# Performance work log

Measured on AMD Instinct MI355X. Metric: run time of the kernel, lower is better.

## Reference

```python
import jax, jax.numpy as jnp
import numpy as np

B, W, H, C = 64, 32, 32, 64
K = 4096  # embedding_length


def setup_inputs() -> dict:
    key = jax.random.key(0)
    k1, k2 = jax.random.split(key)
    encoded = jax.random.normal(k1, (B, W, H, C), dtype=jnp.float32)
    # tf.random.uniform init in the original
    codebook = jax.random.uniform(k2, (K, C), dtype=jnp.float32)
    return {"encoded": encoded, "codebook": codebook}


def reference(encoded, codebook):
    b, w, h, c = encoded.shape
    x = encoded.reshape(b * w * h, c)  # [N, c]
    # the tiled tf.pow(x - e, 2).sum(-1), without the [N, K, c] intermediate).
    x_sq = jnp.sum(x * x, axis=-1, keepdims=True)          # [N, 1]
    e_sq = jnp.sum(codebook * codebook, axis=-1)           # [K]
    dist = x_sq - 2.0 * (x @ codebook.T) + e_sq[None, :]   # [N, K]
    idx = jnp.argmin(dist, axis=-1)                        # [N]
    q = codebook[idx].reshape(b, w, h, c)                  # gather
    # Straight-through estimator as in the original forward
    out = encoded + jax.lax.stop_gradient(q - encoded)
    return out, idx.reshape(b, w, h)
```

## Files before the change

### kernel.cpp

```cpp
#include <hip/hip_runtime.h>


#define NPTS    65536
#define CDIM    64
#define KCODES  4096
#define WAVES   4
#define KPW     (KCODES / WAVES)
#define TILES   (KPW / 16)
#define PADC    64
#define LISTCAP 8192
#define DELTA   0.25f

typedef __attribute__((ext_vector_type(8))) short short8;
typedef __attribute__((ext_vector_type(4))) float f32x4;

__device__ __forceinline__ unsigned short f2bf(float x) {
    unsigned u = __float_as_uint(x);
    return (unsigned short)((u + 0x7FFFu + ((u >> 16) & 1u)) >> 16);
}

struct BT { short8 b0, b1; float hh; };

__global__ __launch_bounds__(256) void vq_prep(const float* __restrict__ cb,
                                               short* __restrict__ cbb,
                                               float* __restrict__ h) {
    int k = blockIdx.x * 256 + threadIdx.x;
    const float4* p = reinterpret_cast<const float4*>(cb + (size_t)k * CDIM);
    float s0 = 0.f, s1 = 0.f, s2 = 0.f, s3 = 0.f;
#pragma unroll
    for (int i = 0; i < 16; i += 2) {
        float4 va = p[i], vb = p[i + 1];
        s0 = fmaf(va.x, va.x, s0); s1 = fmaf(va.y, va.y, s1);
        s2 = fmaf(va.z, va.z, s2); s3 = fmaf(va.w, va.w, s3);
        s0 = fmaf(vb.x, vb.x, s0); s1 = fmaf(vb.y, vb.y, s1);
        s2 = fmaf(vb.z, vb.z, s2); s3 = fmaf(vb.w, vb.w, s3);
        short8 o;
        o[0] = (short)f2bf(va.x); o[1] = (short)f2bf(va.y);
        o[2] = (short)f2bf(va.z); o[3] = (short)f2bf(va.w);
        o[4] = (short)f2bf(vb.x); o[5] = (short)f2bf(vb.y);
        o[6] = (short)f2bf(vb.z); o[7] = (short)f2bf(vb.w);
        *reinterpret_cast<short8*>(cbb + (size_t)k * CDIM + i * 4) = o;
    }
    h[k] = 0.5f * ((s0 + s1) + (s2 + s3));
}

__global__ __launch_bounds__(256) void vq_main(const float* __restrict__ enc,
                                               const float* __restrict__ cbf,
                                               const short* __restrict__ cbb,
                                               const float* __restrict__ h,
                                               float* __restrict__ out) {
    __shared__ unsigned list[LISTCAP];
    __shared__ float rowmax[WAVES][64];
    __shared__ float thrL[64];
    __shared__ unsigned long long mkey[64];
    __shared__ unsigned lcnt;

    const int tid  = threadIdx.x;
    const int wid  = tid >> 6, lane = tid & 63;
    const int lrow = lane & 15, lseg = lane >> 4;
    const int pbase = blockIdx.x * 64;
    const int k0 = wid * KPW;

    if (tid == 0) lcnt = 0;
    if (tid < 64) mkey[tid] = ~0ull;

    short8 afr[4][2];
#pragma unroll
    for (int rt = 0; rt < 4; ++rt)
#pragma unroll
        for (int kk = 0; kk < 2; ++kk) {
            const float4* xp = reinterpret_cast<const float4*>(
                enc + (size_t)(pbase + rt * 16 + lrow) * CDIM + kk * 32 + lseg * 8);
            float4 v0 = xp[0], v1 = xp[1];
            short8 a;
            a[0] = (short)f2bf(v0.x); a[1] = (short)f2bf(v0.y);
            a[2] = (short)f2bf(v0.z); a[3] = (short)f2bf(v0.w);
            a[4] = (short)f2bf(v1.x); a[5] = (short)f2bf(v1.y);
            a[6] = (short)f2bf(v1.z); a[7] = (short)f2bf(v1.w);
            afr[rt][kk] = a;
        }
    __syncthreads();

    auto loadB = [&](int ct, BT& s) {
        int code = k0 + ct * 16 + lrow;
        const short* base = cbb + (size_t)code * CDIM + lseg * 8;
        s.b0 = *reinterpret_cast<const short8*>(base);
        s.b1 = *reinterpret_cast<const short8*>(base + 32);
        s.hh = h[code];
    };

    f32x4 best[4];
#pragma unroll
    for (int rt = 0; rt < 4; ++rt)
#pragma unroll
        for (int i = 0; i < 4; ++i) best[rt][i] = -__builtin_inff();

    {
        BT s0, s1, s2, s3;
        loadB(0, s0); loadB(8, s1); loadB(16, s2); loadB(24, s3);
#define SSBODY(SLOT, J)                                                        \
        {                                                                      \
            float nh = -SLOT.hh;                                               \
            f32x4 acc[4];                                                      \
            _Pragma("unroll")                                                  \
            for (int rt = 0; rt < 4; ++rt) {                                   \
                acc[rt][0] = nh; acc[rt][1] = nh;                              \
                acc[rt][2] = nh; acc[rt][3] = nh;                              \
            }                                                                  \
            _Pragma("unroll")                                                  \
            for (int rt = 0; rt < 4; ++rt)                                     \
                acc[rt] = __builtin_amdgcn_mfma_f32_16x16x32_bf16(afr[rt][0], SLOT.b0, acc[rt], 0, 0, 0); \
            _Pragma("unroll")                                                  \
            for (int rt = 0; rt < 4; ++rt)                                     \
                acc[rt] = __builtin_amdgcn_mfma_f32_16x16x32_bf16(afr[rt][1], SLOT.b1, acc[rt], 0, 0, 0); \
            _Pragma("unroll")                                                  \
            for (int rt = 0; rt < 4; ++rt)                                     \
                _Pragma("unroll")                                              \
                for (int i = 0; i < 4; ++i)                                    \
                    best[rt][i] = fmaxf(best[rt][i], acc[rt][i]);              \
            loadB((((J) + 4) & 7) * 8, SLOT);                                  \
        }
        SSBODY(s0, 0) SSBODY(s1, 1) SSBODY(s2, 2) SSBODY(s3, 3)
        SSBODY(s0, 4) SSBODY(s1, 5) SSBODY(s2, 6) SSBODY(s3, 7)
#undef SSBODY
    }

#pragma unroll
    for (int m = 1; m <= 8; m <<= 1)
#pragma unroll
        for (int rt = 0; rt < 4; ++rt)
#pragma unroll
            for (int i = 0; i < 4; ++i)
                best[rt][i] = fmaxf(best[rt][i], __shfl_xor(best[rt][i], m, 64));
    if (lrow == 0) {
#pragma unroll
        for (int rt = 0; rt < 4; ++rt)
#pragma unroll
            for (int i = 0; i < 4; ++i)
                rowmax[wid][rt * 16 + lseg * 4 + i] = best[rt][i];
    }
    __syncthreads();
    if (tid < 64) {
        float m0 = fmaxf(rowmax[0][tid], rowmax[1][tid]);
        float m1 = fmaxf(rowmax[2][tid], rowmax[3][tid]);
        thrL[tid] = fmaxf(m0, m1) - DELTA;
    }
    __syncthreads();

    f32x4 mthr[4];
#pragma unroll
    for (int rt = 0; rt < 4; ++rt)
#pragma unroll
        for (int i = 0; i < 4; ++i) mthr[rt][i] = -thrL[rt * 16 + lseg * 4 + i];

    {
        BT s0, s1, s2, s3;
        loadB(0, s0); loadB(1, s1); loadB(2, s2); loadB(3, s3);
#define S2BODY(SLOT, T)                                                        \
        {                                                                      \
            f32x4 acc[4];                                                      \
            _Pragma("unroll")                                                  \
            for (int rt = 0; rt < 4; ++rt)                                     \
                acc[rt] = __builtin_amdgcn_mfma_f32_16x16x32_bf16(afr[rt][0], SLOT.b0, mthr[rt], 0, 0, 0); \
            _Pragma("unroll")                                                  \
            for (int rt = 0; rt < 4; ++rt)                                     \
                acc[rt] = __builtin_amdgcn_mfma_f32_16x16x32_bf16(afr[rt][1], SLOT.b1, acc[rt], 0, 0, 0); \
            float hh = SLOT.hh;                                                \
            unsigned mask = 0u;                                                \
            _Pragma("unroll")                                                  \
            for (int rt = 0; rt < 4; ++rt)                                     \
                _Pragma("unroll")                                              \
                for (int i = 0; i < 4; ++i)                                    \
                    mask |= (acc[rt][i] >= hh) ? (1u << (rt * 4 + i)) : 0u;    \
            if (mask) {                                                        \
                unsigned code = (unsigned)(k0 + (T) * 16 + lrow);              \
                do {                                                           \
                    int kz = __builtin_ctz(mask);                              \
                    mask &= mask - 1u;                                         \
                    unsigned row = ((unsigned)(kz >> 2) << 4)                  \
                                 + (unsigned)(lseg * 4) + (unsigned)(kz & 3);   \
                    unsigned pos = atomicAdd(&lcnt, 1u);                       \
                    if (pos < LISTCAP) list[pos] = (row << 12) | code;         \
                } while (mask);                                                \
            }                                                                  \
            loadB((T) + 4, SLOT);           \
        }
        for (int t = 0; t < TILES; t += 4) {
            S2BODY(s0, t + 0)
            S2BODY(s1, t + 1)
            S2BODY(s2, t + 2)
            S2BODY(s3, t + 3)
        }
#undef S2BODY
    }
    __syncthreads();

    unsigned cnt = lcnt; if (cnt > LISTCAP) cnt = LISTCAP;
    for (unsigned t4 = tid; t4 < cnt * 4; t4 += 256) {
        unsigned t = t4 >> 2; int q = t4 & 3;
        unsigned e = list[t];
        int row = (int)(e >> 12), c = (int)(e & 4095u);
        const float4* xp = reinterpret_cast<const float4*>(enc + (size_t)(pbase + row) * CDIM) + q * 4;
        const float4* ep = reinterpret_cast<const float4*>(cbf + (size_t)c * CDIM) + q * 4;
        float a0 = 0.f, a1 = 0.f, a2 = 0.f, a3 = 0.f;
#pragma unroll
        for (int i = 0; i < 4; ++i) {
            float4 xv = xp[i], ev = ep[i];
            a0 = fmaf(xv.x, ev.x, a0); a1 = fmaf(xv.y, ev.y, a1);
            a2 = fmaf(xv.z, ev.z, a2); a3 = fmaf(xv.w, ev.w, a3);
        }
        float p = (a0 + a1) + (a2 + a3);
        p += __shfl_xor(p, 1, 64);
        p += __shfl_xor(p, 2, 64);
        if (q == 0) {
            float d2 = fmaf(-2.f, p, 2.f * h[c]);
            unsigned bb = __float_as_uint(d2);
            unsigned ord = bb ^ (unsigned)(((int)bb >> 31) | 0x80000000);
            atomicMin(&mkey[row], ((unsigned long long)ord << 32) | (unsigned)c);
        }
    }
    __syncthreads();

    {
        int p = tid >> 2, q = tid & 3;
        int c = (int)(mkey[p] & 4095u);
        const float4* ep = reinterpret_cast<const float4*>(cbf + (size_t)c * CDIM) + q * 4;
        float4* op = reinterpret_cast<float4*>(out + (size_t)(pbase + p) * CDIM) + q * 4;
#pragma unroll
        for (int i = 0; i < 4; ++i) op[i] = ep[i];
        if (tid < 64)
            out[(size_t)NPTS * CDIM + pbase + tid] = (float)(mkey[tid] & 4095u);
    }
}

extern "C" void kernel_launch(void* const* d_in, const int* in_sizes, int n_in,
                              void* d_out, int out_size, void* d_ws, size_t ws_size,
                              hipStream_t stream) {
    const float* enc = (const float*)d_in[0];
    const float* cb  = (const float*)d_in[1];
    float* out = (float*)d_out;

    short* cbb = (short*)d_ws;
    float* hws = (float*)(cbb + (size_t)(KCODES + PADC) * CDIM);

    vq_prep<<<KCODES / 256, 256, 0, stream>>>(cb, cbb, hws);
    vq_main<<<NPTS / 64, 256, 0, stream>>>(enc, cb, cbb, hws, out);
}
```

Baseline: 134.0 us.

## Switch to 32x32x16 MFMA tiles with 32 points per block

Replaces the 16x16x32 bf16 MFMA tiling (64 points per block, four row tiles) with 32x32x16 MFMA over 32 points per block and 32 codes per tile, and doubles the grid size. This cuts A-fragment registers and changes the reduction, threshold and row mapping to match the new accumulator layout. The goal is better MFMA throughput per instruction and more blocks for occupancy. The cost is that codebook B fragments are now reloaded by twice as many blocks, and the software pipeline depth drops from four slots to two.

Result: slower. 177.5 us (+32.5%).

```diff
diff --git a/kernel.cpp b/kernel.cpp
--- a/kernel.cpp
+++ b/kernel.cpp
@@ -5,21 +5,22 @@
 #define CDIM    64
 #define KCODES  4096
 #define WAVES   4
+#define PPB     32
 #define KPW     (KCODES / WAVES)
-#define TILES   (KPW / 16)
+#define TILES   (KPW / 32)
 #define PADC    64
-#define LISTCAP 8192
+#define LISTCAP 4096
 #define DELTA   0.25f
 
 typedef __attribute__((ext_vector_type(8))) short short8;
-typedef __attribute__((ext_vector_type(4))) float f32x4;
+typedef __attribute__((ext_vector_type(16))) float f32x16;
 
 __device__ __forceinline__ unsigned short f2bf(float x) {
     unsigned u = __float_as_uint(x);
     return (unsigned short)((u + 0x7FFFu + ((u >> 16) & 1u)) >> 16);
 }
 
-struct BT { short8 b0, b1; float hh; };
+struct BT { short8 b[4]; float hh; };
 
 __global__ __launch_bounds__(256) void vq_prep(const float* __restrict__ cb,
                                                short* __restrict__ cbb,
@@ -50,146 +51,144 @@
                                                const float* __restrict__ h,
                                                float* __restrict__ out) {
     __shared__ unsigned list[LISTCAP];
-    __shared__ float rowmax[WAVES][64];
-    __shared__ float thrL[64];
-    __shared__ unsigned long long mkey[64];
+    __shared__ float rowmax[WAVES][PPB];
+    __shared__ float thrL[PPB];
+    __shared__ unsigned long long mkey[PPB];
     __shared__ unsigned lcnt;
 
     const int tid  = threadIdx.x;
     const int wid  = tid >> 6, lane = tid & 63;
-    const int lrow = lane & 15, lseg = lane >> 4;
-    const int pbase = blockIdx.x * 64;
+    const int col  = lane & 31, hs = lane >> 5;
+    const int pbase = blockIdx.x * PPB;
     const int k0 = wid * KPW;
 
     if (tid == 0) lcnt = 0;
-    if (tid < 64) mkey[tid] = ~0ull;
-
-    short8 afr[4][2];
-#pragma unroll
-    for (int rt = 0; rt < 4; ++rt)
-#pragma unroll
-        for (int kk = 0; kk < 2; ++kk) {
-            const float4* xp = reinterpret_cast<const float4*>(
-                enc + (size_t)(pbase + rt * 16 + lrow) * CDIM + kk * 32 + lseg * 8);
-            float4 v0 = xp[0], v1 = xp[1];
-            short8 a;
-            a[0] = (short)f2bf(v0.x); a[1] = (short)f2bf(v0.y);
-            a[2] = (short)f2bf(v0.z); a[3] = (short)f2bf(v0.w);
-            a[4] = (short)f2bf(v1.x); a[5] = (short)f2bf(v1.y);
-            a[6] = (short)f2bf(v1.z); a[7] = (short)f2bf(v1.w);
-            afr[rt][kk] = a;
-        }
-    __syncthreads();
-
-    auto loadB = [&](int ct, BT& s) {
-        int code = k0 + ct * 16 + lrow;
-        const short* base = cbb + (size_t)code * CDIM + lseg * 8;
-        s.b0 = *reinterpret_cast<const short8*>(base);
-        s.b1 = *reinterpret_cast<const short8*>(base + 32);
+    if (tid < PPB) mkey[tid] = ~0ull;
+
+    short8 afr[4];
+#pragma unroll
+    for (int c = 0; c < 4; ++c) {
+        const float4* xp = reinterpret_cast<const float4*>(
+            enc + (size_t)(pbase + col) * CDIM + c * 16 + hs * 8);
+        float4 v0 = xp[0], v1 = xp[1];
+        short8 a;
+        a[0] = (short)f2bf(v0.x); a[1] = (short)f2bf(v0.y);
+        a[2] = (short)f2bf(v0.z); a[3] = (short)f2bf(v0.w);
+        a[4] = (short)f2bf(v1.x); a[5] = (short)f2bf(v1.y);
+        a[6] = (short)f2bf(v1.z); a[7] = (short)f2bf(v1.w);
+        afr[c] = a;
+    }
+    __syncthreads();
+
+    auto loadB = [&](int t, BT& s) {
+        int code = k0 + t * 32 + col;
+        const short* base = cbb + (size_t)code * CDIM + hs * 8;
+#pragma unroll
+        for (int c = 0; c < 4; ++c)
+            s.b[c] = *reinterpret_cast<const short8*>(base + c * 16);
         s.hh = h[code];
     };
 
-    f32x4 best[4];
-#pragma unroll
-    for (int rt = 0; rt < 4; ++rt)
-#pragma unroll
-        for (int i = 0; i < 4; ++i) best[rt][i] = -__builtin_inff();
+    auto mfmaT = [&](const BT& s, const f32x16& cin) -> f32x16 {
+        f32x16 acc = __builtin_amdgcn_mfma_f32_32x32x16_bf16(afr[0], s.b[0], cin, 0, 0, 0);
+        acc = __builtin_amdgcn_mfma_f32_32x32x16_bf16(afr[1], s.b[1], acc, 0, 0, 0);
+        acc = __builtin_amdgcn_mfma_f32_32x32x16_bf16(afr[2], s.b[2], acc, 0, 0, 0);
+        acc = __builtin_amdgcn_mfma_f32_32x32x16_bf16(afr[3], s.b[3], acc, 0, 0, 0);
+        return acc;
+    };
+
+    float best[16];
+#pragma unroll
+    for (int r = 0; r < 16; ++r) best[r] = -__builtin_inff();
 
     {
-        BT s0, s1, s2, s3;
-        loadB(0, s0); loadB(8, s1); loadB(16, s2); loadB(24, s3);
-#define SSBODY(SLOT, J)                                                        \
-        {                                                                      \
-            float nh = -SLOT.hh;                                               \
-            f32x4 acc[4];                                                      \
-            _Pragma("unroll")                                                  \
-            for (int rt = 0; rt < 4; ++rt) {                                   \
-                acc[rt][0] = nh; acc[rt][1] = nh;                              \
-                acc[rt][2] = nh; acc[rt][3] = nh;                              \
-            }                                                                  \
-            _Pragma("unroll")                                                  \
-            for (int rt = 0; rt < 4; ++rt)                                     \
-                acc[rt] = __builtin_amdgcn_mfma_f32_16x16x32_bf16(afr[rt][0], SLOT.b0, acc[rt], 0, 0, 0); \
-            _Pragma("unroll")                                                  \
-            for (int rt = 0; rt < 4; ++rt)                                     \
-                acc[rt] = __builtin_amdgcn_mfma_f32_16x16x32_bf16(afr[rt][1], SLOT.b1, acc[rt], 0, 0, 0); \
-            _Pragma("unroll")                                                  \
-            for (int rt = 0; rt < 4; ++rt)                                     \
-                _Pragma("unroll")                                              \
-                for (int i = 0; i < 4; ++i)                                    \
-                    best[rt][i] = fmaxf(best[rt][i], acc[rt][i]);              \
-            loadB((((J) + 4) & 7) * 8, SLOT);                                  \
-        }
-        SSBODY(s0, 0) SSBODY(s1, 1) SSBODY(s2, 2) SSBODY(s3, 3)
-        SSBODY(s0, 4) SSBODY(s1, 5) SSBODY(s2, 6) SSBODY(s3, 7)
-#undef SSBODY
-    }
-
-#pragma unroll
-    for (int m = 1; m <= 8; m <<= 1)
-#pragma unroll
-        for (int rt = 0; rt < 4; ++rt)
-#pragma unroll
-            for (int i = 0; i < 4; ++i)
-                best[rt][i] = fmaxf(best[rt][i], __shfl_xor(best[rt][i], m, 64));
-    if (lrow == 0) {
-#pragma unroll
-        for (int rt = 0; rt < 4; ++rt)
-#pragma unroll
-            for (int i = 0; i < 4; ++i)
-                rowmax[wid][rt * 16 + lseg * 4 + i] = best[rt][i];
-    }
-    __syncthreads();
-    if (tid < 64) {
+        BT s0, s1;
+        loadB(0, s0); loadB(8, s1);
+        {
+            f32x16 ci; float nh = -s0.hh;
+#pragma unroll
+            for (int r = 0; r < 16; ++r) ci[r] = nh;
+            f32x16 acc = mfmaT(s0, ci);
+            loadB(16, s0);
+#pragma unroll
+            for (int r = 0; r < 16; ++r) best[r] = fmaxf(best[r], acc[r]);
+        }
+        {
+            f32x16 ci; float nh = -s1.hh;
+#pragma unroll
+            for (int r = 0; r < 16; ++r) ci[r] = nh;
+            f32x16 acc = mfmaT(s1, ci);
+            loadB(24, s1);
+#pragma unroll
+            for (int r = 0; r < 16; ++r) best[r] = fmaxf(best[r], acc[r]);
+        }
+        {
+            f32x16 ci; float nh = -s0.hh;
+#pragma unroll
+            for (int r = 0; r < 16; ++r) ci[r] = nh;
+            f32x16 acc = mfmaT(s0, ci);
+#pragma unroll
+            for (int r = 0; r < 16; ++r) best[r] = fmaxf(best[r], acc[r]);
+        }
+        {
+            f32x16 ci; float nh = -s1.hh;
+#pragma unroll
+            for (int r = 0; r < 16; ++r) ci[r] = nh;
+            f32x16 acc = mfmaT(s1, ci);
+#pragma unroll
+            for (int r = 0; r < 16; ++r) best[r] = fmaxf(best[r], acc[r]);
+        }
+    }
+
+#pragma unroll
+    for (int m = 1; m <= 16; m <<= 1)
+#pragma unroll
+        for (int r = 0; r < 16; ++r)
+            best[r] = fmaxf(best[r], __shfl_xor(best[r], m, 64));
+    if (col == 0) {
+#pragma unroll
+        for (int r = 0; r < 16; ++r)
+            rowmax[wid][(r & 3) + 8 * (r >> 2) + 4 * hs] = best[r];
+    }
+    __syncthreads();
+    if (tid < PPB) {
         float m0 = fmaxf(rowmax[0][tid], rowmax[1][tid]);
         float m1 = fmaxf(rowmax[2][tid], rowmax[3][tid]);
         thrL[tid] = fmaxf(m0, m1) - DELTA;
     }
     __syncthreads();
 
-    f32x4 mthr[4];
-#pragma unroll
-    for (int rt = 0; rt < 4; ++rt)
-#pragma unroll
-        for (int i = 0; i < 4; ++i) mthr[rt][i] = -thrL[rt * 16 + lseg * 4 + i];
+    f32x16 mthr;
+#pragma unroll
+    for (int r = 0; r < 16; ++r)
+        mthr[r] = -thrL[(r & 3) + 8 * (r >> 2) + 4 * hs];
 
     {
-        BT s0, s1, s2, s3;
-        loadB(0, s0); loadB(1, s1); loadB(2, s2); loadB(3, s3);
+        BT s0, s1;
+        loadB(0, s0); loadB(1, s1);
 #define S2BODY(SLOT, T)                                                        \
         {                                                                      \
-            f32x4 acc[4];                                                      \
-            _Pragma("unroll")                                                  \
-            for (int rt = 0; rt < 4; ++rt)                                     \
-                acc[rt] = __builtin_amdgcn_mfma_f32_16x16x32_bf16(afr[rt][0], SLOT.b0, mthr[rt], 0, 0, 0); \
-            _Pragma("unroll")                                                  \
-            for (int rt = 0; rt < 4; ++rt)                                     \
-                acc[rt] = __builtin_amdgcn_mfma_f32_16x16x32_bf16(afr[rt][1], SLOT.b1, acc[rt], 0, 0, 0); \
+            f32x16 acc = mfmaT(SLOT, mthr);                                    \
             float hh = SLOT.hh;                                                \
+            loadB((T) + 2, SLOT);           \
             unsigned mask = 0u;                                                \
             _Pragma("unroll")                                                  \
-            for (int rt = 0; rt < 4; ++rt)                                     \
-                _Pragma("unroll")                                              \
-                for (int i = 0; i < 4; ++i)                                    \
-                    mask |= (acc[rt][i] >= hh) ? (1u << (rt * 4 + i)) : 0u;    \
+            for (int r = 0; r < 16; ++r)                                       \
+                mask |= (acc[r] >= hh) ? (1u << r) : 0u;                       \
             if (mask) {                                                        \
-                unsigned code = (unsigned)(k0 + (T) * 16 + lrow);              \
+                unsigned code = (unsigned)(k0 + (T) * 32 + col);               \
                 do {                                                           \
                     int kz = __builtin_ctz(mask);                              \
                     mask &= mask - 1u;                                         \
-                    unsigned row = ((unsigned)(kz >> 2) << 4)                  \
-                                 + (unsigned)(lseg * 4) + (unsigned)(kz & 3);   \
+                    unsigned row = (unsigned)((kz & 3) + 8 * (kz >> 2) + 4 * hs); \
                     unsigned pos = atomicAdd(&lcnt, 1u);                       \
                     if (pos < LISTCAP) list[pos] = (row << 12) | code;         \
                 } while (mask);                                                \
             }                                                                  \
-            loadB((T) + 4, SLOT);           \
-        }
-        for (int t = 0; t < TILES; t += 4) {
+        }
+        for (int t = 0; t < TILES; t += 2) {
             S2BODY(s0, t + 0)
             S2BODY(s1, t + 1)
-            S2BODY(s2, t + 2)
-            S2BODY(s3, t + 3)
         }
 #undef S2BODY
     }
@@ -222,13 +221,13 @@
     __syncthreads();
 
     {
-        int p = tid >> 2, q = tid & 3;
+        int p = tid >> 3, q = tid & 7;
         int c = (int)(mkey[p] & 4095u);
-        const float4* ep = reinterpret_cast<const float4*>(cbf + (size_t)c * CDIM) + q * 4;
-        float4* op = reinterpret_cast<float4*>(out + (size_t)(pbase + p) * CDIM) + q * 4;
-#pragma unroll
-        for (int i = 0; i < 4; ++i) op[i] = ep[i];
-        if (tid < 64)
+        const float4* ep = reinterpret_cast<const float4*>(cbf + (size_t)c * CDIM);
+        float4* op = reinterpret_cast<float4*>(out + (size_t)(pbase + p) * CDIM);
+        op[q] = ep[q];
+        op[q + 8] = ep[q + 8];
+        if (tid < PPB)
             out[(size_t)NPTS * CDIM + pbase + tid] = (float)(mkey[tid] & 4095u);
     }
 }
@@ -244,5 +243,5 @@
     float* hws = (float*)(cbb + (size_t)(KCODES + PADC) * CDIM);
 
     vq_prep<<<KCODES / 256, 256, 0, stream>>>(cb, cbb, hws);
-    vq_main<<<NPTS / 64, 256, 0, stream>>>(enc, cb, cbb, hws, out);
-}
+    vq_main<<<NPTS / PPB, 256, 0, stream>>>(enc, cb, cbb, hws, out);
+}
```
